# Optimization experiments

Measured on AMD Instinct MI355X. Metric: run time of the kernel, lower is better.

The kernel has to match this reference:

```python
import jax, jax.numpy as jnp
import numpy as np

B, T_TEXT, D, T_TOTAL = 16, 1024, 512, 2048


def setup_inputs() -> dict:
    key = jax.random.key(0)
    k1, k2 = jax.random.split(key)
    enc = jax.random.normal(k1, (B, T_TEXT, D), dtype=jnp.float32)
    dur = jax.random.uniform(k2, (B, T_TEXT), dtype=jnp.float32, minval=0.5, maxval=1.5)
    # rescale so each batch's total duration is exactly T_TOTAL -> round(sum)=T_TOTAL,
    # making T_mel = T_TOTAL + 1 (torch.range(0, max) is inclusive) a static shape.
    dur = dur * (T_TOTAL / jnp.sum(dur, axis=-1, keepdims=True))
    return {"encoder_outputs": enc, "duration": dur, "t_mel": T_TOTAL + 1}


def reference(encoder_outputs, duration, t_mel):
    # encoder_outputs: [B, T_text, D]; duration: [B, T_text]; t_mel: static int
    t_tot = jnp.round(jnp.sum(duration, axis=-1, keepdims=True))      # [B, 1]
    e = jnp.cumsum(duration, axis=-1)                                  # [B, T_text]
    c = e - 0.5 * t_tot                                                # [B, T_text]
    t = jnp.arange(t_mel, dtype=duration.dtype)                        # [T_mel]
    # Gaussian kernel logits over (frame time - center) distances
    logits = -0.1 * (t[None, None, :] - c[:, :, None]) ** 2            # [B, T_text, T_mel]
    # exp / sum-over-text == softmax over axis=1 (numerically stable form)
    w = jax.nn.softmax(logits, axis=1)                                 # [B, T_text, T_mel]
    # w^T @ encoder_outputs  ->  [B, T_mel, D]
    return jnp.einsum('btm,btd->bmd', w, encoder_outputs)
```

## Files before the change

### kernel.cpp

```cpp
#include <hip/hip_runtime.h>
#include <math.h>

#define B_   16
#define TT   1024
#define D_   512
#define TMEL 2049
#define TM   16
#define KB   32
#define NTILE ((TMEL + TM - 1) / TM)

__global__ __launch_bounds__(256) void expand_fused(const float* __restrict__ enc,
                                                    const float* __restrict__ dur,
                                                    float* __restrict__ out) {
    const int b    = blockIdx.y;
    const int tile = blockIdx.x;
    const int m0   = tile * TM;
    const int t    = threadIdx.x;
    const int lane = t & 63;
    const int wid  = t >> 6;

    __shared__ float s_c[TT];
    __shared__ float s_wsum[4];
    __shared__ float s_red[256];
    __shared__ float s_fmax[TM], s_finv[TM];
    __shared__ float s_w[KB * TM];

    float4 v = ((const float4*)(dur + (size_t)b * TT))[t];
    float l0 = v.x;
    float l1 = l0 + v.y;
    float l2 = l1 + v.z;
    float l3 = l2 + v.w;
    float x = l3;
    #pragma unroll
    for (int off = 1; off < 64; off <<= 1) {
        float y = __shfl_up(x, off);
        if (lane >= off) x += y;
    }
    if (lane == 63) s_wsum[wid] = x;
    __syncthreads();
    float w0 = s_wsum[0], w1 = s_wsum[1], w2 = s_wsum[2], w3 = s_wsum[3];
    float tot  = w0 + w1 + w2 + w3;
    float wpre = (wid > 0 ? w0 : 0.f) + (wid > 1 ? w1 : 0.f) + (wid > 2 ? w2 : 0.f);
    float excl = wpre + (x - l3);
    float h = 0.5f * roundf(tot);
    s_c[4*t+0] = excl + l0 - h;
    s_c[4*t+1] = excl + l1 - h;
    s_c[4*t+2] = excl + l2 - h;
    s_c[4*t+3] = excl + l3 - h;
    __syncthreads();

    const int m1c = min(m0 + TM - 1, TMEL - 1);
    const float lo = (float)m0 - 16.f;
    const float hi = (float)m1c + 16.f;
    int a, z, mid;
    a = 0; z = TT; while (a < z) { mid = (a + z) >> 1; if (s_c[mid] <  lo) a = mid + 1; else z = mid; } const int j0  = a;
    a = 0; z = TT; while (a < z) { mid = (a + z) >> 1; if (s_c[mid] <= hi) a = mid + 1; else z = mid; } const int j1  = a;
    a = 0; z = TT; while (a < z) { mid = (a + z) >> 1; if (s_c[mid] < (float)m0)  a = mid + 1; else z = mid; } const int jc0 = a;
    a = 0; z = TT; while (a < z) { mid = (a + z) >> 1; if (s_c[mid] < (float)m1c) a = mid + 1; else z = mid; } const int jc1 = a;
    int ilo = min(j0, jc0 - 8);  if (ilo < 0)  ilo = 0;
    int ihi = max(j1, jc1 + 9);  if (ihi > TT) ihi = TT;

    const int f  = t & 15;
    const int sl = t >> 4;
    const int mmf = min(m0 + f, TMEL - 1);
    const float fm = (float)mmf;
    float lmax = -3.4e38f;
    for (int i = ilo + sl; i < ihi; i += 16) {
        float d = fm - s_c[i];
        lmax = fmaxf(lmax, -0.1f * d * d);
    }
    s_red[t] = lmax;
    __syncthreads();
    #pragma unroll
    for (int st = 128; st >= 16; st >>= 1) {
        if (t < st) s_red[t] = fmaxf(s_red[t], s_red[t + st]);
        __syncthreads();
    }
    if (t < TM) s_fmax[t] = s_red[t];
    __syncthreads();
    const float myfmax = s_fmax[f];
    float lsum = 0.f;
    for (int i = ilo + sl; i < ihi; i += 16) {
        float d = fm - s_c[i];
        lsum += __expf(-0.1f * d * d - myfmax);
    }
    s_red[t] = lsum;
    __syncthreads();
    #pragma unroll
    for (int st = 128; st >= 16; st >>= 1) {
        if (t < st) s_red[t] += s_red[t + st];
        __syncthreads();
    }
    if (t < TM) s_finv[t] = 1.f / s_red[t];
    __syncthreads();

    const int d0 = t * 2;
    float ax[TM], ay[TM];
    #pragma unroll
    for (int m = 0; m < TM; ++m) { ax[m] = 0.f; ay[m] = 0.f; }
    const float* encb = enc + (size_t)b * TT * D_;

    for (int k0 = ilo; k0 < ihi; k0 += KB) {
        const int kn = min(KB, ihi - k0);
        __syncthreads();
        for (int p = t; p < KB * TM; p += 256) {
            const int il = p >> 4;
            const int fr = p & 15;
            float wv = 0.f;
            if (il < kn) {
                const int mf = min(m0 + fr, TMEL - 1);
                float d = (float)mf - s_c[k0 + il];
                wv = __expf(-0.1f * d * d - s_fmax[fr]) * s_finv[fr];
            }
            s_w[p] = wv;
        }
        __syncthreads();
        for (int il = 0; il < kn; ++il) {
            const float2 ev = *(const float2*)(encb + (size_t)(k0 + il) * D_ + d0);
            const float4* swv = (const float4*)(s_w + il * TM);
            #pragma unroll
            for (int q = 0; q < 4; ++q) {
                const float4 wq = swv[q];
                ax[q*4+0] += wq.x * ev.x;  ay[q*4+0] += wq.x * ev.y;
                ax[q*4+1] += wq.y * ev.x;  ay[q*4+1] += wq.y * ev.y;
                ax[q*4+2] += wq.z * ev.x;  ay[q*4+2] += wq.z * ev.y;
                ax[q*4+3] += wq.w * ev.x;  ay[q*4+3] += wq.w * ev.y;
            }
        }
    }

    #pragma unroll
    for (int m = 0; m < TM; ++m) {
        const int mm2 = m0 + m;
        if (mm2 < TMEL) {
            *(float2*)(out + ((size_t)b * TMEL + mm2) * D_ + d0) = make_float2(ax[m], ay[m]);
        }
    }
}

extern "C" void kernel_launch(void* const* d_in, const int* in_sizes, int n_in,
                              void* d_out, int out_size, void* d_ws, size_t ws_size,
                              hipStream_t stream) {
    const float* enc = (const float*)d_in[0];
    const float* dur = (const float*)d_in[1];
    float* out = (float*)d_out;
    (void)d_ws; (void)ws_size;

    dim3 grid(NTILE, B_);
    expand_fused<<<grid, 256, 0, stream>>>(enc, dur, out);
}
```

Baseline: 111.3 us.

## Remap threads to 4-wide D by 8 frames, larger K block, nontemporal stores

Each thread now covers 4 consecutive D columns and half of the 16 frames, so encoder loads become float4 and each thread holds 8 float4 accumulators. Two thread groups now load the same encoder rows, which doubles global/L2 read traffic per tile, while weight reads from LDS per element drop. The K block grows from 32 to 64, the weight fill loop only covers valid rows, and output is written with nontemporal stores to avoid cache pollution.

```diff
diff --git a/kernel.cpp b/kernel.cpp
--- a/kernel.cpp
+++ b/kernel.cpp
@@ -6,8 +6,10 @@
 #define D_   512
 #define TMEL 2049
 #define TM   16
-#define KB   32
+#define KB   64
 #define NTILE ((TMEL + TM - 1) / TM)
+
+typedef float nfloat4 __attribute__((ext_vector_type(4)));
 
 __global__ __launch_bounds__(256) void expand_fused(const float* __restrict__ enc,
                                                     const float* __restrict__ dur,
@@ -94,46 +96,48 @@
     if (t < TM) s_finv[t] = 1.f / s_red[t];
     __syncthreads();
 
-    const int d0 = t * 2;
-    float ax[TM], ay[TM];
+    const int fg = t >> 7;
+    const int dt = t & 127;
+    const int d0 = dt * 4;
+    const int frbase = fg * 8;
+    float4 acc[8];
     #pragma unroll
-    for (int m = 0; m < TM; ++m) { ax[m] = 0.f; ay[m] = 0.f; }
+    for (int j = 0; j < 8; ++j) acc[j] = make_float4(0.f, 0.f, 0.f, 0.f);
     const float* encb = enc + (size_t)b * TT * D_;
 
     for (int k0 = ilo; k0 < ihi; k0 += KB) {
         const int kn = min(KB, ihi - k0);
         __syncthreads();
-        for (int p = t; p < KB * TM; p += 256) {
+        for (int p = t; p < kn * TM; p += 256) {
             const int il = p >> 4;
             const int fr = p & 15;
-            float wv = 0.f;
-            if (il < kn) {
-                const int mf = min(m0 + fr, TMEL - 1);
-                float d = (float)mf - s_c[k0 + il];
-                wv = __expf(-0.1f * d * d - s_fmax[fr]) * s_finv[fr];
-            }
-            s_w[p] = wv;
+            const int mf = min(m0 + fr, TMEL - 1);
+            float d = (float)mf - s_c[k0 + il];
+            s_w[p] = __expf(-0.1f * d * d - s_fmax[fr]) * s_finv[fr];
         }
         __syncthreads();
         for (int il = 0; il < kn; ++il) {
-            const float2 ev = *(const float2*)(encb + (size_t)(k0 + il) * D_ + d0);
-            const float4* swv = (const float4*)(s_w + il * TM);
-            #pragma unroll
-            for (int q = 0; q < 4; ++q) {
-                const float4 wq = swv[q];
-                ax[q*4+0] += wq.x * ev.x;  ay[q*4+0] += wq.x * ev.y;
-                ax[q*4+1] += wq.y * ev.x;  ay[q*4+1] += wq.y * ev.y;
-                ax[q*4+2] += wq.z * ev.x;  ay[q*4+2] += wq.z * ev.y;
-                ax[q*4+3] += wq.w * ev.x;  ay[q*4+3] += wq.w * ev.y;
-            }
+            const float4 ev = *(const float4*)(encb + (size_t)(k0 + il) * D_ + d0);
+            const float4 wa = *(const float4*)(s_w + il * TM + frbase);
+            const float4 wb = *(const float4*)(s_w + il * TM + frbase + 4);
+            acc[0].x += wa.x * ev.x; acc[0].y += wa.x * ev.y; acc[0].z += wa.x * ev.z; acc[0].w += wa.x * ev.w;
+            acc[1].x += wa.y * ev.x; acc[1].y += wa.y * ev.y; acc[1].z += wa.y * ev.z; acc[1].w += wa.y * ev.w;
+            acc[2].x += wa.z * ev.x; acc[2].y += wa.z * ev.y; acc[2].z += wa.z * ev.z; acc[2].w += wa.z * ev.w;
+            acc[3].x += wa.w * ev.x; acc[3].y += wa.w * ev.y; acc[3].z += wa.w * ev.z; acc[3].w += wa.w * ev.w;
+            acc[4].x += wb.x * ev.x; acc[4].y += wb.x * ev.y; acc[4].z += wb.x * ev.z; acc[4].w += wb.x * ev.w;
+            acc[5].x += wb.y * ev.x; acc[5].y += wb.y * ev.y; acc[5].z += wb.y * ev.z; acc[5].w += wb.y * ev.w;
+            acc[6].x += wb.z * ev.x; acc[6].y += wb.z * ev.y; acc[6].z += wb.z * ev.z; acc[6].w += wb.z * ev.w;
+            acc[7].x += wb.w * ev.x; acc[7].y += wb.w * ev.y; acc[7].z += wb.w * ev.z; acc[7].w += wb.w * ev.w;
         }
     }
 
     #pragma unroll
-    for (int m = 0; m < TM; ++m) {
-        const int mm2 = m0 + m;
+    for (int j = 0; j < 8; ++j) {
+        const int mm2 = m0 + frbase + j;
         if (mm2 < TMEL) {
-            *(float2*)(out + ((size_t)b * TMEL + mm2) * D_ + d0) = make_float2(ax[m], ay[m]);
+            nfloat4* dst = (nfloat4*)(out + ((size_t)b * TMEL + mm2) * D_ + d0);
+            nfloat4 av = { acc[j].x, acc[j].y, acc[j].z, acc[j].w };
+            __builtin_nontemporal_store(av, dst);
         }
     }
 }
```

Result: faster. 104.7 us (-5.9%).
